# Kernel optimization log

Hardware: AMD Instinct MI355X
Metric: run time of the kernel (lower is better)

## Reference

```python
import jax, jax.numpy as jnp
import numpy as np

B, S, D, H = 4, 2048, 1024, 16
DH = D // H


def setup_inputs() -> dict:
    key = jax.random.key(0)
    ks = jax.random.split(key, 12)
    s = 0.02
    inp = {
        "q": jax.random.normal(ks[0], (B, S, D), jnp.float32),
        "k": jax.random.normal(ks[1], (B, S, D), jnp.float32),
        "v": jax.random.normal(ks[2], (B, S, D), jnp.float32),
        # causal mask, broadcastable over batch and heads (mask==0 -> -1e9)
        "mask": jnp.tril(jnp.ones((S, S), jnp.int32))[None, None, :, :],
        "wq": jax.random.normal(ks[3], (D, D), jnp.float32) * s,
        "bq": jnp.zeros((D,), jnp.float32),
        "wk": jax.random.normal(ks[4], (D, D), jnp.float32) * s,
        "bk": jnp.zeros((D,), jnp.float32),
        "wv": jax.random.normal(ks[5], (D, D), jnp.float32) * s,
        "bv": jnp.zeros((D,), jnp.float32),
        "wo": jax.random.normal(ks[6], (D, D), jnp.float32) * s,
        "bo": jnp.zeros((D,), jnp.float32),
    }
    return inp


def reference(q, k, v, mask, wq, bq, wk, bk, wv, bv, wo, bo):
    # linear projections (torch Linear: x @ W^T + b)
    qh = (q @ wq.T + bq).reshape(B, S, H, DH).transpose(0, 2, 1, 3)  # [B,H,S,DH]
    kh = (k @ wk.T + bk).reshape(B, S, H, DH).transpose(0, 2, 1, 3)
    vh = (v @ wv.T + bv).reshape(B, S, H, DH).transpose(0, 2, 1, 3)
    scale = 1.0 / jnp.sqrt(jnp.float32(DH))
    score = jnp.einsum("bhqd,bhkd->bhqk", qh, kh) * scale  # [B,H,S,S]
    score = jnp.where(mask == 0, jnp.float32(-1e9), score)
    attn = jax.nn.softmax(score, axis=-1)
    ctx = jnp.einsum("bhqk,bhkd->bhqd", attn, vh)  # [B,H,S,DH]
    ctx = ctx.transpose(0, 2, 1, 3).reshape(B, S, D)
    return ctx @ wo.T + bo
```

## Files before the change

kernel.cpp:

```cpp
#include <hip/hip_runtime.h>
#include <hip/hip_bf16.h>

#define NB 4
#define NS 2048
#define ND 1024
#define NH 16
#define NDH 64
#define E_ 8388608
#define W_ 1048576

typedef __attribute__((ext_vector_type(8))) __bf16 bf16x8;
typedef __attribute__((ext_vector_type(4))) float f32x4;
typedef __attribute__((ext_vector_type(2))) unsigned int u32x2;
typedef unsigned short us16;
typedef unsigned int u32;

__device__ __forceinline__ unsigned short f2bf(float f) {
  union { float f; unsigned u; } v; v.f = f;
  unsigned r = v.u + 0x7FFFu + ((v.u >> 16) & 1u);
  return (unsigned short)(r >> 16);
}

typedef const __attribute__((address_space(1))) unsigned int* gas_t;
typedef __attribute__((address_space(3))) unsigned int* las_t;
__device__ __forceinline__ void gl2lds16(const void* g, void* l) {
  __builtin_amdgcn_global_load_lds((gas_t)g, (las_t)l, 16, 0, 0);
}

__global__ __launch_bounds__(256) void conv_bf16(
    const float* __restrict__ q, const float* __restrict__ k, const float* __restrict__ v,
    const float* __restrict__ wq, const float* __restrict__ wk, const float* __restrict__ wv,
    const float* __restrict__ wo,
    us16* __restrict__ qb, us16* __restrict__ kb, us16* __restrict__ vb,
    us16* __restrict__ wqb, us16* __restrict__ wkb, us16* __restrict__ wvb,
    us16* __restrict__ wob)
{
  int b = blockIdx.x;
  int seg, off;
  if (b < 24576) { seg = b >> 13; off = b & 8191; }
  else { b -= 24576; seg = 3 + (b >> 10); off = b & 1023; }
  const float* s; us16* d;
  switch (seg) {
    case 0: s = q;  d = qb;  break;
    case 1: s = k;  d = kb;  break;
    case 2: s = v;  d = vb;  break;
    case 3: s = wq; d = wqb; break;
    case 4: s = wk; d = wkb; break;
    case 5: s = wv; d = wvb; break;
    default: s = wo; d = wob; break;
  }
  size_t idx = ((size_t)off * 256 + threadIdx.x) * 4;
  float4 f = *(const float4*)(s + idx);
  ushort4 u;
  u.x = f2bf(f.x); u.y = f2bf(f.y); u.z = f2bf(f.z); u.w = f2bf(f.w);
  *(ushort4*)(d + idx) = u;
}

__global__ __launch_bounds__(256, 3) void gemm_proj3(
    const us16* __restrict__ A0, const us16* __restrict__ A1, const us16* __restrict__ A2,
    const us16* __restrict__ W0, const us16* __restrict__ W1, const us16* __restrict__ W2,
    const float* __restrict__ b0, const float* __restrict__ b1, const float* __restrict__ b2,
    us16* __restrict__ o0, us16* __restrict__ o1, us16* __restrict__ o2,
    float qscale, int s0, int s1, int s2)
{
  const int seg = (blockIdx.z == 0) ? s0 : (blockIdx.z == 1) ? s1 : s2;
  const us16* A  = (blockIdx.z == 0) ? A0 : (blockIdx.z == 1) ? A1 : A2;
  const us16* Wt = (blockIdx.z == 0) ? W0 : (blockIdx.z == 1) ? W1 : W2;
  const float* bias = (blockIdx.z == 0) ? b0 : (blockIdx.z == 1) ? b1 : b2;
  us16* out = (blockIdx.z == 0) ? o0 : (blockIdx.z == 1) ? o1 : o2;
  const float scale = (seg == 0) ? qscale : 1.0f;

  __shared__ us16 As[128][64];
  __shared__ us16 Bs[128][64];
  const int tid = threadIdx.x;
  const int lane = tid & 63;
  const int w = tid >> 6;
  const int l15 = lane & 15, quad = lane >> 4;
  const int sw = l15 & 7;
  const int rowBase = blockIdx.x * 128, colBase = blockIdx.y * 128;
  const int srow = w * 32 + (lane >> 3);
  const int cu = (lane & 7) ^ ((lane >> 3) & 7);
  const us16* ga = A  + (size_t)(rowBase + srow) * ND + cu * 8;
  const us16* gb = Wt + (size_t)(colBase + srow) * ND + cu * 8;
  const int wr = (w >> 1) * 64, wc = (w & 1) * 64;

  f32x4 acc[4][4] = {};
  for (int kt = 0; kt < ND; kt += 64) {
    __syncthreads();
    #pragma unroll
    for (int c = 0; c < 4; ++c) {
      gl2lds16(ga + kt + c * 8 * ND, &As[w * 32 + c * 8][0]);
      gl2lds16(gb + kt + c * 8 * ND, &Bs[w * 32 + c * 8][0]);
    }
    __syncthreads();
    #pragma unroll
    for (int ks = 0; ks < 2; ++ks) {
      bf16x8 af[4], bfr[4];
      #pragma unroll
      for (int i = 0; i < 4; ++i)
        af[i]  = *(const bf16x8*)&As[wr + i * 16 + l15][((ks * 4 + quad) ^ sw) * 8];
      #pragma unroll
      for (int j = 0; j < 4; ++j)
        bfr[j] = *(const bf16x8*)&Bs[wc + j * 16 + l15][((ks * 4 + quad) ^ sw) * 8];
      #pragma unroll
      for (int i = 0; i < 4; ++i)
        #pragma unroll
        for (int j = 0; j < 4; ++j)
          acc[i][j] = __builtin_amdgcn_mfma_f32_16x16x32_bf16(af[i], bfr[j], acc[i][j], 0, 0, 0);
    }
  }

  if (seg < 2) {
    #pragma unroll
    for (int i = 0; i < 4; ++i) {
      #pragma unroll
      for (int j = 0; j < 4; ++j) {
        int colg = colBase + wc + j * 16 + l15;
        float bval = bias[colg];
        #pragma unroll
        for (int r = 0; r < 4; ++r) {
          int rowg = rowBase + wr + i * 16 + quad * 4 + r;
          out[(size_t)rowg * ND + colg] = f2bf((acc[i][j][r] + bval) * scale);
        }
      }
    }
  } else {
    #pragma unroll
    for (int i = 0; i < 4; ++i) {
      #pragma unroll
      for (int j = 0; j < 4; ++j) {
        int colg = colBase + wc + j * 16 + l15;
        float bval = bias[colg];
        int h_ = colg >> 6, d_ = colg & 63;
        int rowg0 = rowBase + wr + i * 16 + quad * 4;
        int b_ = rowg0 >> 11, sr0 = rowg0 & (NS - 1);
        ushort4 vv;
        vv.x = f2bf(acc[i][j][0] + bval);
        vv.y = f2bf(acc[i][j][1] + bval);
        vv.z = f2bf(acc[i][j][2] + bval);
        vv.w = f2bf(acc[i][j][3] + bval);
        *(ushort4*)(out + ((size_t)(b_ * NH + h_) * NDH + d_) * NS + sr0) = vv;
      }
    }
  }
}

__global__ __launch_bounds__(512, 2) void attn(
    const us16* __restrict__ Qh, const us16* __restrict__ Kh,
    const us16* __restrict__ Vht, us16* __restrict__ ctx)
{
  __shared__ us16 Ks[2][128][64];
  __shared__ us16 Vts[2][64][128];
  __shared__ us16 Ps[8][16][32];
  us16* Qsta = &Vts[1][0][0];

  const int bh = blockIdx.x & 63;
  const int pr = blockIdx.x >> 6;
  const int b_ = bh >> 4, h_ = bh & 15;
  const int tid = threadIdx.x, lane = tid & 63, w = tid >> 6;
  const int l15 = lane & 15, quad = lane >> 4;
  const int sw = l15 & 7;
  const int lr8 = lane >> 3;
  const int cu = (lane & 7) ^ (lr8 & 7);
  const int vr = lane >> 4;
  const int vs = lane & 15;
  const int cs0 = (vs & 8) | ((vs & 7) ^ vr);
  const int cs1 = (vs & 8) | ((vs & 7) ^ (vr | 4));

  bf16x8 ones;
  #pragma unroll
  for (int i = 0; i < 8; ++i) ones[i] = (__bf16)1.0f;

  const us16* gk  = Kh  + ((size_t)b_ * NS + w * 16 + lr8) * ND + h_ * NDH + cu * 8;
  const us16* gv0 = Vht + ((size_t)bh * NDH + w * 8 + vr) * NS + cs0 * 8;
  const us16* gv1 = Vht + ((size_t)bh * NDH + w * 8 + 4 + vr) * NS + cs1 * 8;

  for (int pass = 0; pass < 2; ++pass) {
    const int tq = pass ? (15 - pr) : pr;
    const int qb0 = tq * 128;
    const int nt = tq + 1;
    const int qw = qb0 + w * 16;

    __syncthreads();
    {
      const us16* gq = Qh + ((size_t)b_ * NS + qb0 + w * 16 + lr8) * ND + h_ * NDH + cu * 8;
      gl2lds16(gq,                    Qsta + (w * 16) * 64);
      gl2lds16(gq + (size_t)8 * ND,   Qsta + (w * 16 + 8) * 64);
    }
    gl2lds16(gk,            &Ks[0][w * 16][0]);
    gl2lds16(gk + 8 * ND,   &Ks[0][w * 16 + 8][0]);
    gl2lds16(gv0,           &Vts[0][w * 8][0]);
    gl2lds16(gv1,           &Vts[0][w * 8 + 4][0]);
    __syncthreads();
    bf16x8 bq[2];
    #pragma unroll
    for (int c = 0; c < 2; ++c)
      bq[c] = *(const bf16x8*)(Qsta + (w * 16 + l15) * 64 + (((c * 4 + quad) ^ sw) * 8));

    f32x4 o[4] = {};
    f32x4 o_l = {};

    for (int it = 0; it < nt; ++it) {
      const int kb = it * 128;
      const int cur = it & 1;
      __syncthreads();
      if (it + 1 < nt) {
        const int nxt = cur ^ 1;
        const int kn = kb + 128;
        gl2lds16(gk + (size_t)kn * ND,        &Ks[nxt][w * 16][0]);
        gl2lds16(gk + (size_t)(kn + 8) * ND,  &Ks[nxt][w * 16 + 8][0]);
        gl2lds16(gv0 + kn,                    &Vts[nxt][w * 8][0]);
        gl2lds16(gv1 + kn,                    &Vts[nxt][w * 8 + 4][0]);
      }
      #pragma unroll
      for (int h2 = 0; h2 < 4; ++h2) {
        const int keyb0 = kb + h2 * 32;
        if (keyb0 > qw + 15) continue;
        const bool full = (keyb0 + 31 <= qw);
        f32x4 s[2];
        __builtin_amdgcn_s_setprio(1);
        #pragma unroll
        for (int mt = 0; mt < 2; ++mt) {
          bf16x8 ak0 = *(const bf16x8*)&Ks[cur][h2 * 32 + mt * 16 + l15][(quad ^ sw) * 8];
          bf16x8 ak1 = *(const bf16x8*)&Ks[cur][h2 * 32 + mt * 16 + l15][((4 + quad) ^ sw) * 8];
          f32x4 t = {};
          t = __builtin_amdgcn_mfma_f32_16x16x32_bf16(ak0, bq[0], t, 0, 0, 0);
          t = __builtin_amdgcn_mfma_f32_16x16x32_bf16(ak1, bq[1], t, 0, 0, 0);
          s[mt] = t;
        }
        __builtin_amdgcn_s_setprio(0);
        #pragma unroll
        for (int mt = 0; mt < 2; ++mt) {
          u32 u[4];
          if (full) {
            #pragma unroll
            for (int r = 0; r < 4; ++r)
              u[r] = __float_as_uint(__builtin_amdgcn_exp2f(s[mt][r]));
          } else {
            const int keyb = keyb0 + mt * 16 + quad * 4;
            const int qg = qw + l15;
            #pragma unroll
            for (int r = 0; r < 4; ++r) {
              float p = (keyb + r <= qg) ? __builtin_amdgcn_exp2f(s[mt][r]) : 0.f;
              u[r] = __float_as_uint(p);
            }
          }
          u32 lo = (u[0] >> 16) | (u[1] & 0xffff0000u);
          u32 hi = (u[2] >> 16) | (u[3] & 0xffff0000u);
          int uswz = (mt * 2 + (quad >> 1)) ^ (l15 & 3);
          *(u32x2*)&Ps[w][l15][uswz * 8 + (quad & 1) * 4] = (u32x2){lo, hi};
        }
        bf16x8 bv[4];
        #pragma unroll
        for (int n = 0; n < 4; ++n)
          bv[n] = *(const bf16x8*)&Vts[cur][n * 16 + l15][((h2 * 4 + quad) ^ sw) * 8];
        __builtin_amdgcn_s_setprio(1);
        {
          bf16x8 ap = *(const bf16x8*)&Ps[w][l15][(quad ^ (l15 & 3)) * 8];
          o_l = __builtin_amdgcn_mfma_f32_16x16x32_bf16(ap, ones, o_l, 0, 0, 0);
          #pragma unroll
          for (int n = 0; n < 4; ++n)
            o[n] = __builtin_amdgcn_mfma_f32_16x16x32_bf16(ap, bv[n], o[n], 0, 0, 0);
        }
        __builtin_amdgcn_s_setprio(0);
      }
    }

    #pragma unroll
    for (int r = 0; r < 4; ++r) {
      float inv = __builtin_amdgcn_rcpf(o_l[r]);
      int qg = qb0 + w * 16 + quad * 4 + r;
      us16* dst = ctx + ((size_t)b_ * NS + qg) * ND + h_ * NDH;
      #pragma unroll
      for (int n = 0; n < 4; ++n)
        dst[n * 16 + l15] = f2bf(o[n][r] * inv);
    }
  }
}

__global__ __launch_bounds__(256, 3) void gemm_out(
    const us16* __restrict__ A, const us16* __restrict__ Wt,
    const float* __restrict__ bias, float* __restrict__ out)
{
  __shared__ us16 As[128][64];
  __shared__ us16 Bs[128][64];
  const int tid = threadIdx.x;
  const int lane = tid & 63;
  const int w = tid >> 6;
  const int l15 = lane & 15, quad = lane >> 4;
  const int sw = l15 & 7;
  const int rowBase = blockIdx.x * 128, colBase = blockIdx.y * 128;
  const int srow = w * 32 + (lane >> 3);
  const int cu = (lane & 7) ^ ((lane >> 3) & 7);
  const us16* ga = A  + (size_t)(rowBase + srow) * ND + cu * 8;
  const us16* gb = Wt + (size_t)(colBase + srow) * ND + cu * 8;
  const int wr = (w >> 1) * 64, wc = (w & 1) * 64;

  f32x4 acc[4][4] = {};
  for (int kt = 0; kt < ND; kt += 64) {
    __syncthreads();
    #pragma unroll
    for (int c = 0; c < 4; ++c) {
      gl2lds16(ga + kt + c * 8 * ND, &As[w * 32 + c * 8][0]);
      gl2lds16(gb + kt + c * 8 * ND, &Bs[w * 32 + c * 8][0]);
    }
    __syncthreads();
    #pragma unroll
    for (int ks = 0; ks < 2; ++ks) {
      bf16x8 af[4], bfr[4];
      #pragma unroll
      for (int i = 0; i < 4; ++i)
        af[i]  = *(const bf16x8*)&As[wr + i * 16 + l15][((ks * 4 + quad) ^ sw) * 8];
      #pragma unroll
      for (int j = 0; j < 4; ++j)
        bfr[j] = *(const bf16x8*)&Bs[wc + j * 16 + l15][((ks * 4 + quad) ^ sw) * 8];
      #pragma unroll
      for (int i = 0; i < 4; ++i)
        #pragma unroll
        for (int j = 0; j < 4; ++j)
          acc[i][j] = __builtin_amdgcn_mfma_f32_16x16x32_bf16(af[i], bfr[j], acc[i][j], 0, 0, 0);
    }
  }

  #pragma unroll
  for (int i = 0; i < 4; ++i) {
    #pragma unroll
    for (int j = 0; j < 4; ++j) {
      int colg = colBase + wc + j * 16 + l15;
      float bval = bias[colg];
      #pragma unroll
      for (int r = 0; r < 4; ++r) {
        int rowg = rowBase + wr + i * 16 + quad * 4 + r;
        out[(size_t)rowg * ND + colg] = acc[i][j][r] + bval;
      }
    }
  }
}

extern "C" void kernel_launch(void* const* d_in, const int* in_sizes, int n_in,
                              void* d_out, int out_size, void* d_ws, size_t ws_size,
                              hipStream_t stream) {
  const float* q  = (const float*)d_in[0];
  const float* k  = (const float*)d_in[1];
  const float* v  = (const float*)d_in[2];
  const float* wq = (const float*)d_in[4];
  const float* bq_ = (const float*)d_in[5];
  const float* wk = (const float*)d_in[6];
  const float* bk_ = (const float*)d_in[7];
  const float* wv = (const float*)d_in[8];
  const float* bv_ = (const float*)d_in[9];
  const float* wo = (const float*)d_in[10];
  const float* bo_ = (const float*)d_in[11];

  us16* ws = (us16*)d_ws;
  us16* qb  = ws;
  us16* kb  = ws + (size_t)E_;
  us16* vb  = ws + (size_t)2 * E_;
  us16* wqb = ws + (size_t)3 * E_;
  us16* wkb = wqb + W_;
  us16* wvb = wkb + W_;
  us16* wob = wvb + W_;
  us16* KhF = wob + W_;
  us16* ctx = vb;
  us16* Vht = (us16*)d_out;
  us16* Qh  = (us16*)d_out + (size_t)E_;

  const float qscale = 0.125f * 1.44269504088896340736f;
  const bool fused = ws_size >= ((size_t)4 * E_ + 4 * W_) * 2;

  conv_bf16<<<28672, 256, 0, stream>>>(q, k, v, wq, wk, wv, wo,
                                       qb, kb, vb, wqb, wkb, wvb, wob);
  if (fused) {
    gemm_proj3<<<dim3(64, 8, 3), 256, 0, stream>>>(
        qb, kb, vb, wqb, wkb, wvb, bq_, bk_, bv_, Qh, KhF, Vht, qscale, 0, 1, 2);
    attn<<<512, 512, 0, stream>>>(Qh, KhF, Vht, ctx);
  } else {
    gemm_proj3<<<dim3(64, 8, 2), 256, 0, stream>>>(
        qb, vb, vb, wqb, wvb, wvb, bq_, bv_, bv_, Qh, Vht, Vht, qscale, 0, 2, 2);
    gemm_proj3<<<dim3(64, 8, 1), 256, 0, stream>>>(
        kb, kb, kb, wkb, wkb, wkb, bk_, bk_, bk_, qb, qb, qb, qscale, 1, 1, 1);
    attn<<<512, 512, 0, stream>>>(Qh, qb, Vht, ctx);
  }
  gemm_out<<<dim3(64, 8), 256, 0, stream>>>(ctx, wob, bo_, (float*)d_out);
}
```

Measured before the change: 297.8 us.

## Switch attention to 32x32x16 MFMA with register-resident P via permlane swaps

Rewrites the attention kernel to use 32x32x16 bf16 MFMAs with 256-query tiles (32 queries per wave), halving the grid to 256 blocks. The P matrix now stays in registers, repacked with cvt_pk_bf16 and permlane32_swap instead of a round trip through LDS. The row sum is accumulated in scalar adds rather than an extra MFMA against a ones vector. Q is loaded straight from global memory into registers. Occupancy drops to one block per CU and the grid is smaller, which risks load imbalance and less latency hiding.

```diff
diff --git a/kernel.cpp b/kernel.cpp
--- a/kernel.cpp
+++ b/kernel.cpp
@@ -11,7 +11,7 @@
 
 typedef __attribute__((ext_vector_type(8))) __bf16 bf16x8;
 typedef __attribute__((ext_vector_type(4))) float f32x4;
-typedef __attribute__((ext_vector_type(2))) unsigned int u32x2;
+typedef __attribute__((ext_vector_type(16))) float f32x16;
 typedef unsigned short us16;
 typedef unsigned int u32;
 
@@ -145,21 +145,20 @@
   }
 }
 
-__global__ __launch_bounds__(512, 2) void attn(
+__global__ __launch_bounds__(512, 1) void attn(
     const us16* __restrict__ Qh, const us16* __restrict__ Kh,
     const us16* __restrict__ Vht, us16* __restrict__ ctx)
 {
   __shared__ us16 Ks[2][128][64];
   __shared__ us16 Vts[2][64][128];
-  __shared__ us16 Ps[8][16][32];
-  us16* Qsta = &Vts[1][0][0];
+  __shared__ float invL[8][32];
 
   const int bh = blockIdx.x & 63;
   const int pr = blockIdx.x >> 6;
   const int b_ = bh >> 4, h_ = bh & 15;
   const int tid = threadIdx.x, lane = tid & 63, w = tid >> 6;
-  const int l15 = lane & 15, quad = lane >> 4;
-  const int sw = l15 & 7;
+  const int l31 = lane & 31;
+  const int hi = lane >> 5;
   const int lr8 = lane >> 3;
   const int cu = (lane & 7) ^ (lr8 & 7);
   const int vr = lane >> 4;
@@ -167,38 +166,33 @@
   const int cs0 = (vs & 8) | ((vs & 7) ^ vr);
   const int cs1 = (vs & 8) | ((vs & 7) ^ (vr | 4));
 
-  bf16x8 ones;
-  #pragma unroll
-  for (int i = 0; i < 8; ++i) ones[i] = (__bf16)1.0f;
-
   const us16* gk  = Kh  + ((size_t)b_ * NS + w * 16 + lr8) * ND + h_ * NDH + cu * 8;
   const us16* gv0 = Vht + ((size_t)bh * NDH + w * 8 + vr) * NS + cs0 * 8;
   const us16* gv1 = Vht + ((size_t)bh * NDH + w * 8 + 4 + vr) * NS + cs1 * 8;
 
   for (int pass = 0; pass < 2; ++pass) {
-    const int tq = pass ? (15 - pr) : pr;
-    const int qb0 = tq * 128;
-    const int nt = tq + 1;
-    const int qw = qb0 + w * 16;
-
-    __syncthreads();
+    const int tq = pass ? (7 - pr) : pr;
+    const int qb0 = tq * 256;
+    const int nt = (tq + 1) * 2;
+    const int qw = qb0 + w * 32;
+    const int qg = qw + l31;
+
+    bf16x8 bq[4];
     {
-      const us16* gq = Qh + ((size_t)b_ * NS + qb0 + w * 16 + lr8) * ND + h_ * NDH + cu * 8;
-      gl2lds16(gq,                    Qsta + (w * 16) * 64);
-      gl2lds16(gq + (size_t)8 * ND,   Qsta + (w * 16 + 8) * 64);
-    }
+      const us16* gq = Qh + ((size_t)b_ * NS + qg) * ND + h_ * NDH + hi * 8;
+      #pragma unroll
+      for (int ds = 0; ds < 4; ++ds)
+        bq[ds] = *(const bf16x8*)(gq + ds * 16);
+    }
+
+    __syncthreads();
     gl2lds16(gk,            &Ks[0][w * 16][0]);
     gl2lds16(gk + 8 * ND,   &Ks[0][w * 16 + 8][0]);
     gl2lds16(gv0,           &Vts[0][w * 8][0]);
     gl2lds16(gv1,           &Vts[0][w * 8 + 4][0]);
-    __syncthreads();
-    bf16x8 bq[2];
-    #pragma unroll
-    for (int c = 0; c < 2; ++c)
-      bq[c] = *(const bf16x8*)(Qsta + (w * 16 + l15) * 64 + (((c * 4 + quad) ^ sw) * 8));
-
-    f32x4 o[4] = {};
-    f32x4 o_l = {};
+
+    f32x16 o0 = {}, o1 = {};
+    float o_l = 0.f;
 
     for (int it = 0; it < nt; ++it) {
       const int kb = it * 128;
@@ -213,67 +207,84 @@
         gl2lds16(gv1 + kn,                    &Vts[nxt][w * 8 + 4][0]);
       }
       #pragma unroll
-      for (int h2 = 0; h2 < 4; ++h2) {
-        const int keyb0 = kb + h2 * 32;
-        if (keyb0 > qw + 15) continue;
+      for (int kb4 = 0; kb4 < 4; ++kb4) {
+        const int keyb0 = kb + kb4 * 32;
+        if (keyb0 > qw + 31) continue;
         const bool full = (keyb0 + 31 <= qw);
-        f32x4 s[2];
+
+        f32x16 c = {};
         __builtin_amdgcn_s_setprio(1);
         #pragma unroll
-        for (int mt = 0; mt < 2; ++mt) {
-          bf16x8 ak0 = *(const bf16x8*)&Ks[cur][h2 * 32 + mt * 16 + l15][(quad ^ sw) * 8];
-          bf16x8 ak1 = *(const bf16x8*)&Ks[cur][h2 * 32 + mt * 16 + l15][((4 + quad) ^ sw) * 8];
-          f32x4 t = {};
-          t = __builtin_amdgcn_mfma_f32_16x16x32_bf16(ak0, bq[0], t, 0, 0, 0);
-          t = __builtin_amdgcn_mfma_f32_16x16x32_bf16(ak1, bq[1], t, 0, 0, 0);
-          s[mt] = t;
+        for (int ds = 0; ds < 4; ++ds) {
+          bf16x8 ak = *(const bf16x8*)
+              &Ks[cur][kb4 * 32 + l31][(((ds * 2 + hi) ^ (l31 & 7)) * 8)];
+          c = __builtin_amdgcn_mfma_f32_32x32x16_bf16(ak, bq[ds], c, 0, 0, 0);
         }
         __builtin_amdgcn_s_setprio(0);
-        #pragma unroll
-        for (int mt = 0; mt < 2; ++mt) {
-          u32 u[4];
-          if (full) {
-            #pragma unroll
-            for (int r = 0; r < 4; ++r)
-              u[r] = __float_as_uint(__builtin_amdgcn_exp2f(s[mt][r]));
-          } else {
-            const int keyb = keyb0 + mt * 16 + quad * 4;
-            const int qg = qw + l15;
-            #pragma unroll
-            for (int r = 0; r < 4; ++r) {
-              float p = (keyb + r <= qg) ? __builtin_amdgcn_exp2f(s[mt][r]) : 0.f;
-              u[r] = __float_as_uint(p);
-            }
+
+        float p[16];
+        if (full) {
+          #pragma unroll
+          for (int r = 0; r < 16; ++r)
+            p[r] = __builtin_amdgcn_exp2f(c[r]);
+        } else {
+          #pragma unroll
+          for (int r = 0; r < 16; ++r) {
+            int kg = keyb0 + (r & 3) + 8 * (r >> 2) + 4 * hi;
+            p[r] = (kg <= qg) ? __builtin_amdgcn_exp2f(c[r]) : 0.f;
           }
-          u32 lo = (u[0] >> 16) | (u[1] & 0xffff0000u);
-          u32 hi = (u[2] >> 16) | (u[3] & 0xffff0000u);
-          int uswz = (mt * 2 + (quad >> 1)) ^ (l15 & 3);
-          *(u32x2*)&Ps[w][l15][uswz * 8 + (quad & 1) * 4] = (u32x2){lo, hi};
         }
-        bf16x8 bv[4];
-        #pragma unroll
-        for (int n = 0; n < 4; ++n)
-          bv[n] = *(const bf16x8*)&Vts[cur][n * 16 + l15][((h2 * 4 + quad) ^ sw) * 8];
+        {
+          float s0 = (p[0] + p[1]) + (p[2] + p[3]);
+          float s1 = (p[4] + p[5]) + (p[6] + p[7]);
+          float s2 = (p[8] + p[9]) + (p[10] + p[11]);
+          float s3 = (p[12] + p[13]) + (p[14] + p[15]);
+          o_l += (s0 + s1) + (s2 + s3);
+        }
+        u32 m[8];
+        #pragma unroll
+        for (int j = 0; j < 8; ++j)
+          asm("v_cvt_pk_bf16_f32 %0, %1, %2" : "=v"(m[j]) : "v"(p[2 * j]), "v"(p[2 * j + 1]));
+        asm volatile("v_permlane32_swap_b32 %0, %1" : "+v"(m[0]), "+v"(m[2]));
+        asm volatile("v_permlane32_swap_b32 %0, %1" : "+v"(m[1]), "+v"(m[3]));
+        asm volatile("v_permlane32_swap_b32 %0, %1" : "+v"(m[4]), "+v"(m[6]));
+        asm volatile("v_permlane32_swap_b32 %0, %1" : "+v"(m[5]), "+v"(m[7]));
+        union { u32 u[4]; bf16x8 v; } pa0, pa1;
+        pa0.u[0] = m[0]; pa0.u[1] = m[1]; pa0.u[2] = m[2]; pa0.u[3] = m[3];
+        pa1.u[0] = m[4]; pa1.u[1] = m[5]; pa1.u[2] = m[6]; pa1.u[3] = m[7];
+
+        const int sw7 = l31 & 7;
+        const int g0 = kb4 * 4 + hi;
+        const int g1 = kb4 * 4 + 2 + hi;
+        const int s00 = (g0 & 8) | ((g0 & 7) ^ sw7);
+        const int s01 = (g1 & 8) | ((g1 & 7) ^ sw7);
+        bf16x8 bv00 = *(const bf16x8*)&Vts[cur][l31][s00 * 8];
+        bf16x8 bv01 = *(const bf16x8*)&Vts[cur][l31][s01 * 8];
+        bf16x8 bv10 = *(const bf16x8*)&Vts[cur][32 + l31][s00 * 8];
+        bf16x8 bv11 = *(const bf16x8*)&Vts[cur][32 + l31][s01 * 8];
         __builtin_amdgcn_s_setprio(1);
-        {
-          bf16x8 ap = *(const bf16x8*)&Ps[w][l15][(quad ^ (l15 & 3)) * 8];
-          o_l = __builtin_amdgcn_mfma_f32_16x16x32_bf16(ap, ones, o_l, 0, 0, 0);
-          #pragma unroll
-          for (int n = 0; n < 4; ++n)
-            o[n] = __builtin_amdgcn_mfma_f32_16x16x32_bf16(ap, bv[n], o[n], 0, 0, 0);
-        }
+        o0 = __builtin_amdgcn_mfma_f32_32x32x16_bf16(pa0.v, bv00, o0, 0, 0, 0);
+        o0 = __builtin_amdgcn_mfma_f32_32x32x16_bf16(pa1.v, bv01, o0, 0, 0, 0);
+        o1 = __builtin_amdgcn_mfma_f32_32x32x16_bf16(pa0.v, bv10, o1, 0, 0, 0);
+        o1 = __builtin_amdgcn_mfma_f32_32x32x16_bf16(pa1.v, bv11, o1, 0, 0, 0);
         __builtin_amdgcn_s_setprio(0);
       }
     }
 
-    #pragma unroll
-    for (int r = 0; r < 4; ++r) {
-      float inv = __builtin_amdgcn_rcpf(o_l[r]);
-      int qg = qb0 + w * 16 + quad * 4 + r;
-      us16* dst = ctx + ((size_t)b_ * NS + qg) * ND + h_ * NDH;
-      #pragma unroll
-      for (int n = 0; n < 4; ++n)
-        dst[n * 16 + l15] = f2bf(o[n][r] * inv);
+    {
+      float a = o_l, b = o_l;
+      asm volatile("v_permlane32_swap_b32 %0, %1" : "+v"(a), "+v"(b));
+      float tot = a + b;
+      float inv = __builtin_amdgcn_rcpf(tot);
+      if (lane < 32) invL[w][l31] = inv;
+      #pragma unroll
+      for (int r = 0; r < 16; ++r) {
+        int qrow = (r & 3) + 8 * (r >> 2) + 4 * hi;
+        float iv = invL[w][qrow];
+        us16* dst = ctx + ((size_t)b_ * NS + qb0 + w * 32 + qrow) * ND + h_ * NDH + l31;
+        dst[0]  = f2bf(o0[r] * iv);
+        dst[32] = f2bf(o1[r] * iv);
+      }
     }
   }
 }
@@ -373,13 +384,13 @@
   if (fused) {
     gemm_proj3<<<dim3(64, 8, 3), 256, 0, stream>>>(
         qb, kb, vb, wqb, wkb, wvb, bq_, bk_, bv_, Qh, KhF, Vht, qscale, 0, 1, 2);
-    attn<<<512, 512, 0, stream>>>(Qh, KhF, Vht, ctx);
+    attn<<<256, 512, 0, stream>>>(Qh, KhF, Vht, ctx);
   } else {
     gemm_proj3<<<dim3(64, 8, 2), 256, 0, stream>>>(
         qb, vb, vb, wqb, wvb, wvb, bq_, bv_, bv_, Qh, Vht, Vht, qscale, 0, 2, 2);
     gemm_proj3<<<dim3(64, 8, 1), 256, 0, stream>>>(
         kb, kb, kb, wkb, wkb, wkb, bk_, bk_, bk_, qb, qb, qb, qscale, 1, 1, 1);
-    attn<<<512, 512, 0, stream>>>(Qh, qb, Vht, ctx);
+    attn<<<256, 512, 0, stream>>>(Qh, qb, Vht, ctx);
   }
   gemm_out<<<dim3(64, 8), 256, 0, stream>>>(ctx, wob, bo_, (float*)d_out);
 }
```

Result: no change. 299.8 us (+0.7%).
